# Performance work log

Measured on AMD Instinct MI355X. Metric: run time of the kernel, lower is better.

## Reference

```python
import jax, jax.numpy as jnp
import numpy as np

ROPE_BASE = 10000.0


def rotate_half(x):
    # interleaved rotate: (x0,x1,x2,x3,...) -> (-x1,x0,-x3,x2,...)
    x1 = x[..., ::2]
    x2 = x[..., 1::2]
    return jnp.stack((-x2, x1), axis=-1).reshape(x.shape)


def rope_cos_sin(seq_len, dim, dtype):
    inv_freq = 1.0 / (ROPE_BASE ** (jnp.arange(0, dim, 2, dtype=jnp.float32) / dim))
    pos = jnp.arange(seq_len, dtype=jnp.float32)
    freqs = jnp.outer(pos, inv_freq)              # [S, dim/2]
    emb = jnp.concatenate([freqs, freqs], axis=-1)  # [S, dim]
    return jnp.cos(emb).astype(dtype), jnp.sin(emb).astype(dtype)


def setup_inputs() -> dict:
    key = jax.random.key(0)
    k1, k2, k3, k4 = jax.random.split(key, 4)
    B, S, D = 4, 4096, 256
    scale = 1.0 / np.sqrt(D)
    x = jax.random.normal(k1, (B, S, D), dtype=jnp.float32)
    wq = jax.random.normal(k2, (D, D), dtype=jnp.float32) * scale
    wk = jax.random.normal(k3, (D, D), dtype=jnp.float32) * scale
    wv = jax.random.normal(k4, (D, D), dtype=jnp.float32) * scale
    return {"x": x, "wq": wq, "wk": wk, "wv": wv}


def reference(x, wq, wk, wv):
    D = x.shape[-1]
    S = x.shape[-2]
    # torch Linear: y = x @ W^T
    q = jnp.einsum('bsd,ed->bse', x, wq)
    k = jnp.einsum('bsd,ed->bse', x, wk)
    v = jnp.einsum('bsd,ed->bse', x, wv)
    cos, sin = rope_cos_sin(S, D, x.dtype)  # [S, D]
    q = q * cos + rotate_half(q) * sin
    k = k * cos + rotate_half(k) * sin
    scores = jnp.einsum('bqd,bkd->bqk', q, k) / jnp.sqrt(jnp.asarray(D, x.dtype))
    weights = jax.nn.softmax(scores, axis=-1)
    output = jnp.einsum('bqk,bkd->bqd', weights, v)
    return output, weights
```

## Files before the change

kernel.cpp:

```cpp
#include <hip/hip_runtime.h>
#include <hip/hip_bf16.h>
#include <stdint.h>


#define B_ 4
#define S_ 4096
#define D_ 256
#define NQ 4194304
#define NW 65536
#define NTAB 524288

typedef __attribute__((ext_vector_type(4))) float f32x4;
typedef __attribute__((ext_vector_type(8))) short short8;
typedef __attribute__((ext_vector_type(4))) short short4v;
typedef __attribute__((ext_vector_type(4))) unsigned uint32x4;

__device__ __forceinline__ short f2bf(float f) {
  unsigned u = __builtin_bit_cast(unsigned, f);
  u += 0x7fffu + ((u >> 16) & 1u);
  return (short)(u >> 16);
}
__device__ __forceinline__ float bf2f(short h) {
  unsigned u = ((unsigned)(unsigned short)h) << 16;
  return __builtin_bit_cast(float, u);
}

__device__ __forceinline__ void gload16(const void* g, void* l) {
  __builtin_amdgcn_global_load_lds(
      (const __attribute__((address_space(1))) unsigned*)g,
      (__attribute__((address_space(3))) unsigned*)l, 16, 0, 0);
}

__global__ __launch_bounds__(256) void k0_split(
    const float* __restrict__ x, const float* __restrict__ wq,
    const float* __restrict__ wk, const float* __restrict__ wv,
    short* __restrict__ xh, short* __restrict__ xl,
    short* __restrict__ wh, short* __restrict__ wl,
    float* __restrict__ ctab) {
  int idx = blockIdx.x * 256 + threadIdx.x;
  if (idx < NQ) {
    float v = x[idx];
    short hi = f2bf(v);
    xh[idx] = hi;
    xl[idx] = f2bf(v - bf2f(hi));
  } else if (idx < NQ + 3 * NW) {
    int r = idx - NQ;
    int m = r >> 16;
    int e = r & (NW - 1);
    const float* w = (m == 0) ? wq : (m == 1) ? wk : wv;
    float v = w[e];
    short hi = f2bf(v);
    wh[r] = hi;
    wl[r] = f2bf(v - bf2f(hi));
  } else {
    int t = idx - NQ - 3 * NW;
    int s = t >> 7, j = t & 127;
    float invf = __expf(-0.07195578415606394f * (float)j);
    float sn, cs;
    sincosf((float)s * invf, &sn, &cs);
    ctab[2 * t] = cs;
    ctab[2 * t + 1] = sn;
  }
}

__global__ __launch_bounds__(256) void k1_proj(
    const short* __restrict__ xh, const short* __restrict__ xl,
    const short* __restrict__ wh, const short* __restrict__ wl,
    const float* __restrict__ ctab,
    short* __restrict__ qh, short* __restrict__ ql,
    short* __restrict__ kh, short* __restrict__ kl,
    short* __restrict__ vt) {
  const int m = blockIdx.y;
  const int b = blockIdx.x >> 6;
  const int sbase = (blockIdx.x & 63) << 6;
  const int tid = threadIdx.x;
  const int w = tid >> 6;
  const int lane = tid & 63;
  const int lr = lane & 15;
  const int g = lane >> 4;

  const int srow = sbase + w * 16 + lr;
  const short* xhp = xh + ((size_t)(b * S_ + srow)) * D_;
  const short* xlp = xl + ((size_t)(b * S_ + srow)) * D_;
  const short* whm = wh + m * NW;
  const short* wlm = wl + m * NW;

  f32x4 acc[16];
#pragma unroll
  for (int i = 0; i < 16; ++i) acc[i] = (f32x4)0.f;

#pragma unroll
  for (int dc = 0; dc < 8; ++dc) {
    const int d = dc * 32 + g * 8;
    short8 ah = *(const short8*)(xhp + d);
    short8 al = *(const short8*)(xlp + d);
#pragma unroll
    for (int ct = 0; ct < 16; ++ct) {
      const int e = ct * 16 + lr;
      short8 bh = *(const short8*)(whm + e * D_ + d);
      short8 bl = *(const short8*)(wlm + e * D_ + d);
      acc[ct] = __builtin_amdgcn_mfma_f32_16x16x32_bf16(ah, bh, acc[ct], 0, 0, 0);
      acc[ct] = __builtin_amdgcn_mfma_f32_16x16x32_bf16(ah, bl, acc[ct], 0, 0, 0);
      acc[ct] = __builtin_amdgcn_mfma_f32_16x16x32_bf16(al, bh, acc[ct], 0, 0, 0);
    }
  }

  const int s0 = sbase + w * 16 + g * 4;
  if (m == 2) {
#pragma unroll
    for (int ct = 0; ct < 16; ++ct) {
      const int e = ct * 16 + lr;
      short4v pk;
#pragma unroll
      for (int r = 0; r < 4; ++r) pk[r] = f2bf(acc[ct][r]);
      *(short4v*)(vt + ((size_t)(b * D_ + e)) * S_ + s0) = pk;
    }
  } else {
    short* oh = (m == 0) ? qh : kh;
    short* ol = (m == 0) ? ql : kl;
#pragma unroll
    for (int ct = 0; ct < 16; ++ct) {
      const int e = ct * 16 + lr;
      const float sgn = (e & 1) ? 1.0f : -1.0f;
#pragma unroll
      for (int r = 0; r < 4; ++r) {
        float v = acc[ct][r];
        float p = __shfl_xor(v, 1, 64);
        const float2 cs2 = *(const float2*)(ctab + ((size_t)((s0 + r) << 7) + (e & 127)) * 2);
        float q2 = v * cs2.x + sgn * p * cs2.y;
        short hi = f2bf(q2);
        size_t off = ((size_t)(b * S_ + s0 + r)) * D_ + e;
        oh[off] = hi;
        ol[off] = f2bf(q2 - bf2f(hi));
      }
    }
  }
}

__global__ __launch_bounds__(512, 2) void k2_fused(
    const short* __restrict__ qh, const short* __restrict__ ql,
    const short* __restrict__ kh, const short* __restrict__ kl,
    const short* __restrict__ vt,
    float* __restrict__ wts, float* __restrict__ out) {
  __shared__ __align__(16) char kbuf[131072];
  __shared__ __align__(16) char etile[2][8192];
  __shared__ float part[4][64];
  __shared__ float lsum_l[64];

  const int bid = blockIdx.x;
  const int swz = (bid & 7) * 32 + (bid >> 3);
  const int b = swz >> 6;
  const int qbase = (swz & 63) << 6;
  const int tid = threadIdx.x;
  const int w = tid >> 6;
  const int lane = tid & 63;
  const int lr = lane & 15;
  const int g = lane >> 4;
  const int wq2 = w & 1;
  const int wk4 = w >> 1;
  const int qh_pv = w & 1;
  const int dh_pv = w >> 1;

  short8 qfh[2][8], qfl[2][8];
#pragma unroll
  for (int qt = 0; qt < 2; ++qt) {
    const int qrow = qbase + wq2 * 32 + qt * 16 + lr;
    const short* ph = qh + ((size_t)(b * S_ + qrow)) * D_;
    const short* pl = ql + ((size_t)(b * S_ + qrow)) * D_;
#pragma unroll
    for (int dc = 0; dc < 8; ++dc) {
      qfh[qt][dc] = *(const short8*)(ph + dc * 32 + g * 8);
      qfl[qt][dc] = *(const short8*)(pl + dc * 32 + g * 8);
    }
  }

  f32x4 acc[2];
  acc[0] = (f32x4)0.f; acc[1] = (f32x4)0.f;
  f32x4 accv[2][4];
#pragma unroll
  for (int qt = 0; qt < 2; ++qt)
#pragma unroll
    for (int dt = 0; dt < 4; ++dt) accv[qt][dt] = (f32x4)0.f;
  float rs[2] = {0.f, 0.f};

  const char* khb = (const char*)(kh + (size_t)b * S_ * D_);
  const char* klb = (const char*)(kl + (size_t)b * S_ * D_);
  const short* vtb = vt + (size_t)b * D_ * S_;
  const int keyl = wk4 * 16 + lr;
  const int swx = (lane & 7) << 4;

  char* WB = (char*)(wts + ((size_t)(b * S_ + qbase)) * S_);
  char* EB = WB + 524288;

#pragma unroll
  for (int i = 0; i < 4; ++i) {
    const int p = i * 8192 + tid * 16;
    const int xo = p ^ (((p >> 9) & 7) << 4);
    gload16(khb + xo, kbuf + p);
    gload16(klb + xo, kbuf + 32768 + p);
  }
  __syncthreads();

  for (int kt = 0; kt < 64; ++kt) {
    const int cur = kt & 1;
    const char* kb = kbuf + cur * 65536;

    if (kt < 63) {
      const char* sh = khb + (size_t)(kt + 1) * 32768;
      const char* sl = klb + (size_t)(kt + 1) * 32768;
      char* kn = kbuf + (cur ^ 1) * 65536;
#pragma unroll
      for (int i = 0; i < 4; ++i) {
        const int p = i * 8192 + tid * 16;
        const int xo = p ^ (((p >> 9) & 7) << 4);
        gload16(sh + xo, kn + p);
        gload16(sl + xo, kn + 32768 + p);
      }
    }

    if (kt > 0) {
      const char* et = etile[cur ^ 1];
      {
        const int p = tid * 16;
        const int row = p >> 7, cb = p & 127;
        uint32x4 v = *(const uint32x4*)(et + (p ^ ((row & 7) << 4)));
        *(uint32x4*)(EB + (size_t)row * 8192 + (kt - 1) * 128 + cb) = v;
      }
      __builtin_amdgcn_s_setprio(1);
#pragma unroll
      for (int kk = 0; kk < 2; ++kk) {
        short8 ea0, ea1;
        {
          const int row = qh_pv * 32 + lr;
          ea0 = *(const short8*)(et + ((row * 128 + kk * 64 + g * 16) ^ ((row & 7) << 4)));
        }
        {
          const int row = qh_pv * 32 + 16 + lr;
          ea1 = *(const short8*)(et + ((row * 128 + kk * 64 + g * 16) ^ ((row & 7) << 4)));
        }
#pragma unroll
        for (int dt = 0; dt < 4; ++dt) {
          const int d = dh_pv * 64 + dt * 16 + lr;
          short8 vb = *(const short8*)(vtb + (size_t)d * S_ + (kt - 1) * 64 + kk * 32 + g * 8);
          accv[0][dt] = __builtin_amdgcn_mfma_f32_16x16x32_bf16(ea0, vb, accv[0][dt], 0, 0, 0);
          accv[1][dt] = __builtin_amdgcn_mfma_f32_16x16x32_bf16(ea1, vb, accv[1][dt], 0, 0, 0);
        }
      }
      __builtin_amdgcn_s_setprio(0);
    }

    __builtin_amdgcn_s_setprio(1);
#pragma unroll
    for (int dc = 0; dc < 8; ++dc) {
      const int x = (keyl * 512 + dc * 64 + g * 16) ^ swx;
      short8 afh = *(const short8*)(kb + x);
      short8 afl = *(const short8*)(kb + 32768 + x);
      acc[0] = __builtin_amdgcn_mfma_f32_16x16x32_bf16(afh, qfh[0][dc], acc[0], 0, 0, 0);
      acc[0] = __builtin_amdgcn_mfma_f32_16x16x32_bf16(afh, qfl[0][dc], acc[0], 0, 0, 0);
      acc[0] = __builtin_amdgcn_mfma_f32_16x16x32_bf16(afl, qfh[0][dc], acc[0], 0, 0, 0);
      acc[1] = __builtin_amdgcn_mfma_f32_16x16x32_bf16(afh, qfh[1][dc], acc[1], 0, 0, 0);
      acc[1] = __builtin_amdgcn_mfma_f32_16x16x32_bf16(afh, qfl[1][dc], acc[1], 0, 0, 0);
      acc[1] = __builtin_amdgcn_mfma_f32_16x16x32_bf16(afl, qfh[1][dc], acc[1], 0, 0, 0);
    }
    __builtin_amdgcn_s_setprio(0);

#pragma unroll
    for (int qt = 0; qt < 2; ++qt) {
      f32x4 e;
#pragma unroll
      for (int r = 0; r < 4; ++r) e[r] = __expf(acc[qt][r] * 0.0625f);
      rs[qt] += e[0] + e[1] + e[2] + e[3];
      unsigned lo = (unsigned)(unsigned short)f2bf(e[0]) |
                    ((unsigned)(unsigned short)f2bf(e[1]) << 16);
      unsigned hi2 = (unsigned)(unsigned short)f2bf(e[2]) |
                     ((unsigned)(unsigned short)f2bf(e[3]) << 16);
      const int row = wq2 * 32 + qt * 16 + lr;
      const int colb = (wk4 * 16 + g * 4) * 2;
      const int ad = (row * 128 + colb) ^ ((row & 7) << 4);
      *(uint2*)(etile[cur] + ad) = make_uint2(lo, hi2);
      acc[qt] = (f32x4)0.f;
    }
    __syncthreads();
  }

  {
    const char* et = etile[1];
    {
      const int p = tid * 16;
      const int row = p >> 7, cb = p & 127;
      uint32x4 v = *(const uint32x4*)(et + (p ^ ((row & 7) << 4)));
      *(uint32x4*)(EB + (size_t)row * 8192 + 63 * 128 + cb) = v;
    }
#pragma unroll
    for (int kk = 0; kk < 2; ++kk) {
      short8 ea0, ea1;
      {
        const int row = qh_pv * 32 + lr;
        ea0 = *(const short8*)(et + ((row * 128 + kk * 64 + g * 16) ^ ((row & 7) << 4)));
      }
      {
        const int row = qh_pv * 32 + 16 + lr;
        ea1 = *(const short8*)(et + ((row * 128 + kk * 64 + g * 16) ^ ((row & 7) << 4)));
      }
#pragma unroll
      for (int dt = 0; dt < 4; ++dt) {
        const int d = dh_pv * 64 + dt * 16 + lr;
        short8 vb = *(const short8*)(vtb + (size_t)d * S_ + 63 * 64 + kk * 32 + g * 8);
        accv[0][dt] = __builtin_amdgcn_mfma_f32_16x16x32_bf16(ea0, vb, accv[0][dt], 0, 0, 0);
        accv[1][dt] = __builtin_amdgcn_mfma_f32_16x16x32_bf16(ea1, vb, accv[1][dt], 0, 0, 0);
      }
    }
  }

#pragma unroll
  for (int qt = 0; qt < 2; ++qt) {
    rs[qt] += __shfl_xor(rs[qt], 16, 64);
    rs[qt] += __shfl_xor(rs[qt], 32, 64);
  }
  if (lane < 16) {
    part[wk4][wq2 * 32 + lane] = rs[0];
    part[wk4][wq2 * 32 + 16 + lane] = rs[1];
  }
  __syncthreads();
  if (tid < 64)
    lsum_l[tid] = part[0][tid] + part[1][tid] + part[2][tid] + part[3][tid];
  __syncthreads();

#pragma unroll
  for (int i = 0; i < 2; ++i) {
    const int p = i * 8192 + tid * 16;
    *(uint32x4*)(kbuf + p) = *(const uint32x4*)(EB + (size_t)62 * 8192 + p);
  }

  {
    float* ob = out + (size_t)b * S_ * D_;
    float rv[2][4];
#pragma unroll
    for (int qt = 0; qt < 2; ++qt)
#pragma unroll
      for (int r = 0; r < 4; ++r)
        rv[qt][r] = 1.0f / lsum_l[qh_pv * 32 + qt * 16 + g * 4 + r];
#pragma unroll
    for (int qt = 0; qt < 2; ++qt)
#pragma unroll
      for (int dt = 0; dt < 4; ++dt)
#pragma unroll
        for (int r = 0; r < 4; ++r) {
          const int q = qbase + qh_pv * 32 + qt * 16 + g * 4 + r;
          ob[(size_t)q * D_ + dh_pv * 64 + dt * 16 + lr] = accv[qt][dt][r] * rv[qt][r];
        }
  }
  __syncthreads();

  const int pr0[6] = {0, 32, 48, 56, 60, 62};
  const int pr1[6] = {32, 48, 56, 60, 62, 64};
#pragma unroll 1
  for (int ph = 0; ph < 6; ++ph) {
    for (int r = pr0[ph] + w; r < pr1[ph]; r += 8) {
      const float rinv = 1.0f / lsum_l[r];
      const short* erow = (r >= 62) ? (const short*)(kbuf + (size_t)(r - 62) * 8192)
                                    : (const short*)(EB + (size_t)r * 8192);
      float* wrow = (float*)(WB + (size_t)r * 16384);
      for (int c = lane * 8; c < 4096; c += 512) {
        short8 ev = *(const short8*)(erow + c);
        f32x4 o0, o1;
#pragma unroll
        for (int j = 0; j < 4; ++j) o0[j] = bf2f(ev[j]) * rinv;
#pragma unroll
        for (int j = 0; j < 4; ++j) o1[j] = bf2f(ev[4 + j]) * rinv;
        *(f32x4*)(wrow + c) = o0;
        *(f32x4*)(wrow + c + 4) = o1;
      }
    }
    __syncthreads();
  }
}

extern "C" void kernel_launch(void* const* d_in, const int* in_sizes, int n_in,
                              void* d_out, int out_size, void* d_ws, size_t ws_size,
                              hipStream_t stream) {
  const float* x  = (const float*)d_in[0];
  const float* wq = (const float*)d_in[1];
  const float* wk = (const float*)d_in[2];
  const float* wv = (const float*)d_in[3];

  float* out = (float*)d_out;
  float* wts = out + (size_t)B_ * S_ * D_;

  short* xh = (short*)d_ws;
  short* xl = xh + NQ;
  short* qh = xl + NQ;
  short* ql = qh + NQ;
  short* kh = ql + NQ;
  short* kl = kh + NQ;
  short* vt = kl + NQ;
  short* wh = vt + NQ;
  short* wl = wh + 3 * NW;
  float* ctab = (float*)(wl + 3 * NW);

  k0_split<<<dim3((NQ + 3 * NW + NTAB) / 256), 256, 0, stream>>>(
      x, wq, wk, wv, xh, xl, wh, wl, ctab);
  k1_proj<<<dim3(B_ * S_ / 64, 3), 256, 0, stream>>>(
      xh, xl, wh, wl, ctab, qh, ql, kh, kl, vt);
  k2_fused<<<dim3(B_ * S_ / 64), 512, 0, stream>>>(
      qh, ql, kh, kl, vt, wts, out);
}
```

Measured before the change: 473.6 us.

## Split attention key range across two blocks and add separate normalization kernel

The fused attention kernel is split into k2a, which processes half of the keys per block (512 blocks instead of 256), and k2b, which combines partial PV outputs and row sums, then normalizes and expands the bf16 exponent scratch into fp32 weights. This raises parallelism and occupancy (smaller LDS footprint, launch bounds 512,4), and it moves the serialized weight-expansion tail into its own kernel. In exchange it adds an extra launch, writes partial outputs and row sums through global scratch (partials stored in the weights buffer), and has to handle in-place aliasing between the bf16 staging area and the fp32 output.

```diff
diff --git a/kernel.cpp b/kernel.cpp
--- a/kernel.cpp
+++ b/kernel.cpp
@@ -29,6 +29,23 @@
   __builtin_amdgcn_global_load_lds(
       (const __attribute__((address_space(1))) unsigned*)g,
       (__attribute__((address_space(3))) unsigned*)l, 16, 0, 0);
+}
+
+__device__ __forceinline__ void cvt16(const char* er, float* wr, int k0, float rinv) {
+  short8 ev0 = *(const short8*)(er + (size_t)k0 * 2);
+  short8 ev1 = *(const short8*)(er + (size_t)k0 * 2 + 16);
+  f32x4 o0, o1, o2, o3;
+#pragma unroll
+  for (int j = 0; j < 4; ++j) {
+    o0[j] = bf2f(ev0[j]) * rinv;
+    o1[j] = bf2f(ev0[4 + j]) * rinv;
+    o2[j] = bf2f(ev1[j]) * rinv;
+    o3[j] = bf2f(ev1[4 + j]) * rinv;
+  }
+  *(f32x4*)(wr + k0) = o0;
+  *(f32x4*)(wr + k0 + 4) = o1;
+  *(f32x4*)(wr + k0 + 8) = o2;
+  *(f32x4*)(wr + k0 + 12) = o3;
 }
 
 __global__ __launch_bounds__(256) void k0_split(
@@ -137,114 +154,100 @@
   }
 }
 
-__global__ __launch_bounds__(512, 2) void k2_fused(
+__global__ __launch_bounds__(512, 4) void k2a(
     const short* __restrict__ qh, const short* __restrict__ ql,
     const short* __restrict__ kh, const short* __restrict__ kl,
     const short* __restrict__ vt,
-    float* __restrict__ wts, float* __restrict__ out) {
-  __shared__ __align__(16) char kbuf[131072];
-  __shared__ __align__(16) char etile[2][8192];
-  __shared__ float part[4][64];
-  __shared__ float lsum_l[64];
+    float* __restrict__ wts, float* __restrict__ lsum_g) {
+  __shared__ __align__(16) char kbuf[65536];
+  __shared__ __align__(16) char etile[2][4096];
+  __shared__ float part[2][64];
 
   const int bid = blockIdx.x;
-  const int swz = (bid & 7) * 32 + (bid >> 3);
-  const int b = swz >> 6;
-  const int qbase = (swz & 63) << 6;
+  const int grp = bid & 7;
+  const int b = grp >> 1;
+  const int khalf = grp & 1;
+  const int qbase = (bid >> 3) << 6;
   const int tid = threadIdx.x;
   const int w = tid >> 6;
   const int lane = tid & 63;
   const int lr = lane & 15;
   const int g = lane >> 4;
-  const int wq2 = w & 1;
-  const int wk4 = w >> 1;
-  const int qh_pv = w & 1;
-  const int dh_pv = w >> 1;
-
-  short8 qfh[2][8], qfl[2][8];
-#pragma unroll
-  for (int qt = 0; qt < 2; ++qt) {
-    const int qrow = qbase + wq2 * 32 + qt * 16 + lr;
+  const int qg = w & 3;
+  const int wk2 = w >> 2;
+  const int dh = w >> 2;
+
+  short8 qfh[8], qfl[8];
+  {
+    const int qrow = qbase + qg * 16 + lr;
     const short* ph = qh + ((size_t)(b * S_ + qrow)) * D_;
     const short* pl = ql + ((size_t)(b * S_ + qrow)) * D_;
 #pragma unroll
     for (int dc = 0; dc < 8; ++dc) {
-      qfh[qt][dc] = *(const short8*)(ph + dc * 32 + g * 8);
-      qfl[qt][dc] = *(const short8*)(pl + dc * 32 + g * 8);
-    }
-  }
-
-  f32x4 acc[2];
-  acc[0] = (f32x4)0.f; acc[1] = (f32x4)0.f;
-  f32x4 accv[2][4];
-#pragma unroll
-  for (int qt = 0; qt < 2; ++qt)
-#pragma unroll
-    for (int dt = 0; dt < 4; ++dt) accv[qt][dt] = (f32x4)0.f;
-  float rs[2] = {0.f, 0.f};
-
-  const char* khb = (const char*)(kh + (size_t)b * S_ * D_);
-  const char* klb = (const char*)(kl + (size_t)b * S_ * D_);
+      qfh[dc] = *(const short8*)(ph + dc * 32 + g * 8);
+      qfl[dc] = *(const short8*)(pl + dc * 32 + g * 8);
+    }
+  }
+
+  f32x4 acc = (f32x4)0.f;
+  f32x4 accv[8];
+#pragma unroll
+  for (int i = 0; i < 8; ++i) accv[i] = (f32x4)0.f;
+  float rs = 0.f;
+
+  const char* khb = (const char*)(kh + ((size_t)b * S_ + khalf * 2048) * D_);
+  const char* klb = (const char*)(kl + ((size_t)b * S_ + khalf * 2048) * D_);
   const short* vtb = vt + (size_t)b * D_ * S_;
-  const int keyl = wk4 * 16 + lr;
+  const int keyl = wk2 * 16 + lr;
   const int swx = (lane & 7) << 4;
 
-  char* WB = (char*)(wts + ((size_t)(b * S_ + qbase)) * S_);
-  char* EB = WB + 524288;
-
-#pragma unroll
-  for (int i = 0; i < 4; ++i) {
+  float* WBf = wts + ((size_t)(b * S_ + qbase)) * S_;
+  char* EB = (char*)WBf + 524288;
+
+#pragma unroll
+  for (int i = 0; i < 2; ++i) {
     const int p = i * 8192 + tid * 16;
     const int xo = p ^ (((p >> 9) & 7) << 4);
     gload16(khb + xo, kbuf + p);
-    gload16(klb + xo, kbuf + 32768 + p);
+    gload16(klb + xo, kbuf + 16384 + p);
   }
   __syncthreads();
 
   for (int kt = 0; kt < 64; ++kt) {
     const int cur = kt & 1;
-    const char* kb = kbuf + cur * 65536;
+    const char* kb = kbuf + cur * 32768;
 
     if (kt < 63) {
-      const char* sh = khb + (size_t)(kt + 1) * 32768;
-      const char* sl = klb + (size_t)(kt + 1) * 32768;
-      char* kn = kbuf + (cur ^ 1) * 65536;
-#pragma unroll
-      for (int i = 0; i < 4; ++i) {
+      const char* sh = khb + (size_t)(kt + 1) * 16384;
+      const char* sl = klb + (size_t)(kt + 1) * 16384;
+      char* kn = kbuf + (cur ^ 1) * 32768;
+#pragma unroll
+      for (int i = 0; i < 2; ++i) {
         const int p = i * 8192 + tid * 16;
         const int xo = p ^ (((p >> 9) & 7) << 4);
         gload16(sh + xo, kn + p);
-        gload16(sl + xo, kn + 32768 + p);
+        gload16(sl + xo, kn + 16384 + p);
       }
     }
 
     if (kt > 0) {
       const char* et = etile[cur ^ 1];
       {
-        const int p = tid * 16;
-        const int row = p >> 7, cb = p & 127;
-        uint32x4 v = *(const uint32x4*)(et + (p ^ ((row & 7) << 4)));
-        *(uint32x4*)(EB + (size_t)row * 8192 + (kt - 1) * 128 + cb) = v;
+        const int row = tid >> 3, cb = (tid & 7) * 8;
+        uint2 v = *(const uint2*)(et + (row * 64 + (cb ^ ((row & 3) << 4))));
+        *(uint2*)(EB + (size_t)row * 8192 + khalf * 4096 + (kt - 1) * 64 + cb) = v;
       }
       __builtin_amdgcn_s_setprio(1);
-#pragma unroll
-      for (int kk = 0; kk < 2; ++kk) {
-        short8 ea0, ea1;
-        {
-          const int row = qh_pv * 32 + lr;
-          ea0 = *(const short8*)(et + ((row * 128 + kk * 64 + g * 16) ^ ((row & 7) << 4)));
-        }
-        {
-          const int row = qh_pv * 32 + 16 + lr;
-          ea1 = *(const short8*)(et + ((row * 128 + kk * 64 + g * 16) ^ ((row & 7) << 4)));
-        }
-#pragma unroll
-        for (int dt = 0; dt < 4; ++dt) {
-          const int d = dh_pv * 64 + dt * 16 + lr;
-          short8 vb = *(const short8*)(vtb + (size_t)d * S_ + (kt - 1) * 64 + kk * 32 + g * 8);
-          accv[0][dt] = __builtin_amdgcn_mfma_f32_16x16x32_bf16(ea0, vb, accv[0][dt], 0, 0, 0);
-          accv[1][dt] = __builtin_amdgcn_mfma_f32_16x16x32_bf16(ea1, vb, accv[1][dt], 0, 0, 0);
-        }
+      short8 ea;
+      {
+        const int row = qg * 16 + lr;
+        ea = *(const short8*)(et + (row * 64 + ((g * 16) ^ ((row & 3) << 4))));
+      }
+#pragma unroll
+      for (int dt = 0; dt < 8; ++dt) {
+        const int d = dh * 128 + dt * 16 + lr;
+        short8 vb = *(const short8*)(vtb + (size_t)d * S_ + khalf * 2048 + (kt - 1) * 32 + g * 8);
+        accv[dt] = __builtin_amdgcn_mfma_f32_16x16x32_bf16(ea, vb, accv[dt], 0, 0, 0);
       }
       __builtin_amdgcn_s_setprio(0);
     }
@@ -254,31 +257,26 @@
     for (int dc = 0; dc < 8; ++dc) {
       const int x = (keyl * 512 + dc * 64 + g * 16) ^ swx;
       short8 afh = *(const short8*)(kb + x);
-      short8 afl = *(const short8*)(kb + 32768 + x);
-      acc[0] = __builtin_amdgcn_mfma_f32_16x16x32_bf16(afh, qfh[0][dc], acc[0], 0, 0, 0);
-      acc[0] = __builtin_amdgcn_mfma_f32_16x16x32_bf16(afh, qfl[0][dc], acc[0], 0, 0, 0);
-      acc[0] = __builtin_amdgcn_mfma_f32_16x16x32_bf16(afl, qfh[0][dc], acc[0], 0, 0, 0);
-      acc[1] = __builtin_amdgcn_mfma_f32_16x16x32_bf16(afh, qfh[1][dc], acc[1], 0, 0, 0);
-      acc[1] = __builtin_amdgcn_mfma_f32_16x16x32_bf16(afh, qfl[1][dc], acc[1], 0, 0, 0);
-      acc[1] = __builtin_amdgcn_mfma_f32_16x16x32_bf16(afl, qfh[1][dc], acc[1], 0, 0, 0);
+      short8 afl = *(const short8*)(kb + 16384 + x);
+      acc = __builtin_amdgcn_mfma_f32_16x16x32_bf16(afh, qfh[dc], acc, 0, 0, 0);
+      acc = __builtin_amdgcn_mfma_f32_16x16x32_bf16(afh, qfl[dc], acc, 0, 0, 0);
+      acc = __builtin_amdgcn_mfma_f32_16x16x32_bf16(afl, qfh[dc], acc, 0, 0, 0);
     }
     __builtin_amdgcn_s_setprio(0);
 
-#pragma unroll
-    for (int qt = 0; qt < 2; ++qt) {
+    {
       f32x4 e;
 #pragma unroll
-      for (int r = 0; r < 4; ++r) e[r] = __expf(acc[qt][r] * 0.0625f);
-      rs[qt] += e[0] + e[1] + e[2] + e[3];
+      for (int r = 0; r < 4; ++r) e[r] = __expf(acc[r] * 0.0625f);
+      rs += e[0] + e[1] + e[2] + e[3];
       unsigned lo = (unsigned)(unsigned short)f2bf(e[0]) |
                     ((unsigned)(unsigned short)f2bf(e[1]) << 16);
       unsigned hi2 = (unsigned)(unsigned short)f2bf(e[2]) |
                      ((unsigned)(unsigned short)f2bf(e[3]) << 16);
-      const int row = wq2 * 32 + qt * 16 + lr;
-      const int colb = (wk4 * 16 + g * 4) * 2;
-      const int ad = (row * 128 + colb) ^ ((row & 7) << 4);
-      *(uint2*)(etile[cur] + ad) = make_uint2(lo, hi2);
-      acc[qt] = (f32x4)0.f;
+      const int row = qg * 16 + lr;
+      const int cb = (wk2 * 16 + g * 4) * 2;
+      *(uint2*)(etile[cur] + (row * 64 + (cb ^ ((row & 3) << 4)))) = make_uint2(lo, hi2);
+      acc = (f32x4)0.f;
     }
     __syncthreads();
   }
@@ -286,93 +284,119 @@
   {
     const char* et = etile[1];
     {
-      const int p = tid * 16;
-      const int row = p >> 7, cb = p & 127;
-      uint32x4 v = *(const uint32x4*)(et + (p ^ ((row & 7) << 4)));
-      *(uint32x4*)(EB + (size_t)row * 8192 + 63 * 128 + cb) = v;
-    }
-#pragma unroll
-    for (int kk = 0; kk < 2; ++kk) {
-      short8 ea0, ea1;
-      {
-        const int row = qh_pv * 32 + lr;
-        ea0 = *(const short8*)(et + ((row * 128 + kk * 64 + g * 16) ^ ((row & 7) << 4)));
-      }
-      {
-        const int row = qh_pv * 32 + 16 + lr;
-        ea1 = *(const short8*)(et + ((row * 128 + kk * 64 + g * 16) ^ ((row & 7) << 4)));
-      }
-#pragma unroll
-      for (int dt = 0; dt < 4; ++dt) {
-        const int d = dh_pv * 64 + dt * 16 + lr;
-        short8 vb = *(const short8*)(vtb + (size_t)d * S_ + 63 * 64 + kk * 32 + g * 8);
-        accv[0][dt] = __builtin_amdgcn_mfma_f32_16x16x32_bf16(ea0, vb, accv[0][dt], 0, 0, 0);
-        accv[1][dt] = __builtin_amdgcn_mfma_f32_16x16x32_bf16(ea1, vb, accv[1][dt], 0, 0, 0);
-      }
-    }
-  }
-
-#pragma unroll
-  for (int qt = 0; qt < 2; ++qt) {
-    rs[qt] += __shfl_xor(rs[qt], 16, 64);
-    rs[qt] += __shfl_xor(rs[qt], 32, 64);
-  }
-  if (lane < 16) {
-    part[wk4][wq2 * 32 + lane] = rs[0];
-    part[wk4][wq2 * 32 + 16 + lane] = rs[1];
-  }
+      const int row = tid >> 3, cb = (tid & 7) * 8;
+      uint2 v = *(const uint2*)(et + (row * 64 + (cb ^ ((row & 3) << 4))));
+      *(uint2*)(EB + (size_t)row * 8192 + khalf * 4096 + 63 * 64 + cb) = v;
+    }
+    short8 ea;
+    {
+      const int row = qg * 16 + lr;
+      ea = *(const short8*)(et + (row * 64 + ((g * 16) ^ ((row & 3) << 4))));
+    }
+#pragma unroll
+    for (int dt = 0; dt < 8; ++dt) {
+      const int d = dh * 128 + dt * 16 + lr;
+      short8 vb = *(const short8*)(vtb + (size_t)d * S_ + khalf * 2048 + 63 * 32 + g * 8);
+      accv[dt] = __builtin_amdgcn_mfma_f32_16x16x32_bf16(ea, vb, accv[dt], 0, 0, 0);
+    }
+  }
+
+  rs += __shfl_xor(rs, 16, 64);
+  rs += __shfl_xor(rs, 32, 64);
+  if (lane < 16) part[wk2][qg * 16 + lane] = rs;
   __syncthreads();
   if (tid < 64)
-    lsum_l[tid] = part[0][tid] + part[1][tid] + part[2][tid] + part[3][tid];
-  __syncthreads();
-
-#pragma unroll
-  for (int i = 0; i < 2; ++i) {
-    const int p = i * 8192 + tid * 16;
-    *(uint32x4*)(kbuf + p) = *(const uint32x4*)(EB + (size_t)62 * 8192 + p);
-  }
-
-  {
-    float* ob = out + (size_t)b * S_ * D_;
-    float rv[2][4];
-#pragma unroll
-    for (int qt = 0; qt < 2; ++qt)
-#pragma unroll
-      for (int r = 0; r < 4; ++r)
-        rv[qt][r] = 1.0f / lsum_l[qh_pv * 32 + qt * 16 + g * 4 + r];
-#pragma unroll
-    for (int qt = 0; qt < 2; ++qt)
-#pragma unroll
-      for (int dt = 0; dt < 4; ++dt)
-#pragma unroll
-        for (int r = 0; r < 4; ++r) {
-          const int q = qbase + qh_pv * 32 + qt * 16 + g * 4 + r;
-          ob[(size_t)q * D_ + dh_pv * 64 + dt * 16 + lr] = accv[qt][dt][r] * rv[qt][r];
-        }
-  }
-  __syncthreads();
-
-  const int pr0[6] = {0, 32, 48, 56, 60, 62};
-  const int pr1[6] = {32, 48, 56, 60, 62, 64};
-#pragma unroll 1
-  for (int ph = 0; ph < 6; ++ph) {
-    for (int r = pr0[ph] + w; r < pr1[ph]; r += 8) {
-      const float rinv = 1.0f / lsum_l[r];
-      const short* erow = (r >= 62) ? (const short*)(kbuf + (size_t)(r - 62) * 8192)
-                                    : (const short*)(EB + (size_t)r * 8192);
-      float* wrow = (float*)(WB + (size_t)r * 16384);
-      for (int c = lane * 8; c < 4096; c += 512) {
-        short8 ev = *(const short8*)(erow + c);
-        f32x4 o0, o1;
-#pragma unroll
-        for (int j = 0; j < 4; ++j) o0[j] = bf2f(ev[j]) * rinv;
-#pragma unroll
-        for (int j = 0; j < 4; ++j) o1[j] = bf2f(ev[4 + j]) * rinv;
-        *(f32x4*)(wrow + c) = o0;
-        *(f32x4*)(wrow + c + 4) = o1;
-      }
-    }
-    __syncthreads();
+    lsum_g[khalf * 16384 + b * S_ + qbase + tid] = part[0][tid] + part[1][tid];
+
+  {
+    float* pob = WBf + khalf * 16384;
+#pragma unroll
+    for (int dt = 0; dt < 8; ++dt) {
+      const int d = dh * 128 + dt * 16 + lr;
+#pragma unroll
+      for (int r = 0; r < 4; ++r) {
+        const int q = qg * 16 + g * 4 + r;
+        pob[q * 256 + d] = accv[dt][r];
+      }
+    }
+  }
+}
+
+__global__ __launch_bounds__(512) void k2b(
+    float* __restrict__ wts, const float* __restrict__ lsum_g,
+    float* __restrict__ out) {
+  __shared__ float lsum_l[64];
+  __shared__ __align__(16) char ebuf[131072];
+
+  const int bid = blockIdx.x;
+  const int b = bid >> 6;
+  const int qbase = (bid & 63) << 6;
+  const int tid = threadIdx.x;
+
+  float* WBf = wts + ((size_t)(b * S_ + qbase)) * S_;
+  char* WB = (char*)WBf;
+  const char* EB = WB + 524288;
+
+  if (tid < 64)
+    lsum_l[tid] = lsum_g[b * S_ + qbase + tid] + lsum_g[16384 + b * S_ + qbase + tid];
+  __syncthreads();
+
+  {
+    const int q = tid >> 3;
+    const int dg = (tid & 7) * 32;
+    const float rinv = 1.0f / lsum_l[q];
+    const float* po0 = WBf + q * 256 + dg;
+    const float* po1 = po0 + 16384;
+    float* ob = out + ((size_t)(b * S_ + qbase + q)) * D_ + dg;
+#pragma unroll
+    for (int i = 0; i < 8; ++i) {
+      f32x4 a = *(const f32x4*)(po0 + i * 4);
+      f32x4 c = *(const f32x4*)(po1 + i * 4);
+#pragma unroll
+      for (int j = 0; j < 4; ++j) a[j] = (a[j] + c[j]) * rinv;
+      *(f32x4*)(ob + i * 4) = a;
+    }
+#pragma unroll
+    for (int i = 0; i < 16; ++i) {
+      const int p = i * 8192 + tid * 16;
+      *(uint32x4*)(ebuf + p) = *(const uint32x4*)(EB + (size_t)48 * 8192 + p);
+    }
+  }
+  __syncthreads();
+
+  {
+    const int row = tid >> 4;
+    const int ch = tid & 15;
+    const float rinv = 1.0f / lsum_l[row];
+    const char* er = EB + (size_t)row * 8192;
+    float* wr = WBf + (size_t)row * 4096;
+#pragma unroll 2
+    for (int cc = 0; cc < 16; ++cc)
+      cvt16(er, wr, cc * 256 + ch * 16, rinv);
+  }
+  __syncthreads();
+
+  {
+    const int row = 32 + (tid >> 5);
+    const int ch = tid & 31;
+    const float rinv = 1.0f / lsum_l[row];
+    const char* er = EB + (size_t)row * 8192;
+    float* wr = WBf + (size_t)row * 4096;
+#pragma unroll 2
+    for (int cc = 0; cc < 8; ++cc)
+      cvt16(er, wr, cc * 512 + ch * 16, rinv);
+  }
+  __syncthreads();
+
+  {
+    const int row = 48 + (tid >> 5);
+    const int ch = tid & 31;
+    const float rinv = 1.0f / lsum_l[row];
+    const char* er = ebuf + (size_t)(row - 48) * 8192;
+    float* wr = WBf + (size_t)row * 4096;
+#pragma unroll 2
+    for (int cc = 0; cc < 8; ++cc)
+      cvt16(er, wr, cc * 512 + ch * 16, rinv);
   }
 }
 
@@ -397,11 +421,14 @@
   short* wh = vt + NQ;
   short* wl = wh + 3 * NW;
   float* ctab = (float*)(wl + 3 * NW);
+  float* lsum_g = ctab + 2 * NTAB;
 
   k0_split<<<dim3((NQ + 3 * NW + NTAB) / 256), 256, 0, stream>>>(
       x, wq, wk, wv, xh, xl, wh, wl, ctab);
   k1_proj<<<dim3(B_ * S_ / 64, 3), 256, 0, stream>>>(
       xh, xl, wh, wl, ctab, qh, ql, kh, kl, vt);
-  k2_fused<<<dim3(B_ * S_ / 64), 512, 0, stream>>>(
-      qh, ql, kh, kl, vt, wts, out);
-}
+  k2a<<<dim3(512), 512, 0, stream>>>(
+      qh, ql, kh, kl, vt, wts, lsum_g);
+  k2b<<<dim3(256), 512, 0, stream>>>(
+      wts, lsum_g, out);
+}
```

Result: slower. 664.5 us (+40.3%).
